# Kernel optimization log

Measured on AMD Instinct MI355X. Metric: run time of the kernel, lower is better.

Reference implementation:

```python
import jax, jax.numpy as jnp
import numpy as np

B, N, K, F, E = 2, 16384, 32, 64, 16


def setup_inputs() -> dict:
    key = jax.random.key(0)
    k1, k2, k3, k4 = jax.random.split(key, 4)
    nodes = jax.random.normal(k1, (B, N, F), dtype=jnp.float32)
    # neighbor list: for each (batch, node) a list of K neighbor node indices
    nlist = jax.random.randint(k2, (B, N, K), 0, N, dtype=jnp.int32)
    edges = jax.random.normal(k3, (B, N, K, E), dtype=jnp.float32)
    # learned weight: (node_feat, node_feat, edge_feat) as in build()
    w = jax.random.normal(k4, (F, F, E), dtype=jnp.float32) * 0.05
    return {"nodes": nodes, "nlist": nlist, "edges": edges, "w": w}


def reference(nodes, nlist, edges, w):
    # tf.gather_nd(nodes, nlist): gather neighbor features -> [B, N, K, F]
    batch_idx = jnp.arange(nodes.shape[0], dtype=nlist.dtype)[:, None, None]
    sliced = nodes[batch_idx, nlist]  # [B, N, K, F]
    # edge-conditioned contraction: edges[b,i,j,n] * sliced[b,i,j,l] * w[l,m,n]
    prod = jnp.einsum('bijn,bijl,lmn->bijm', edges, sliced, w)  # [B, N, K, F]
    # mean over the K neighbors (axis=2); activation is None
    reduced = jnp.mean(prod, axis=2)  # [B, N, F]
    return reduced
```

## Files before the change

kernel.cpp:

```cpp
#include <hip/hip_runtime.h>
#include <cstdint>
#include <cstddef>

#define LOGN 14

typedef __bf16 bf16x8 __attribute__((ext_vector_type(8)));
typedef float f32x4 __attribute__((ext_vector_type(4)));
typedef unsigned u32;

#define BARRIER() __builtin_amdgcn_s_barrier()
#define LGKM0()   __builtin_amdgcn_s_waitcnt(0xC07F)
#define SFENCE()  __builtin_amdgcn_sched_barrier(0)

__device__ __forceinline__ u32 fbits(float f) { return __builtin_bit_cast(u32, f); }
__device__ __forceinline__ u32 pkrne(float lo, float hi) {
  u32 a = fbits(lo); a = a + 0x7fffu + ((a >> 16) & 1u);
  u32 b = fbits(hi); b = b + 0x7fffu + ((b >> 16) & 1u);
  return (b & 0xffff0000u) | (a >> 16);
}


__global__ void prep_wt(const float* __restrict__ w, unsigned short* __restrict__ wt) {
  int idx = blockIdx.x * 256 + threadIdx.x;
  int m = idx >> 10, k = idx & 1023;
  int ch = k >> 3, wv = k & 7, t = ch >> 4, cc = ch & 15;
  int l = (cc << 2) + (t >> 1), n = ((t & 1) << 3) + wv;
  u32 u = fbits(w[l * 1024 + m * 16 + n] * 0.03125f);
  wt[idx] = (unsigned short)((u + 0x7fffu + ((u >> 16) & 1u)) >> 16);
}

__device__ __forceinline__ bf16x8 mk_bw(const float* wp) {
  float v[8];
  #pragma unroll
  for (int i = 0; i < 8; ++i) v[i] = wp[i] * 0.03125f;
  uint4 pk{pkrne(v[0], v[1]), pkrne(v[2], v[3]), pkrne(v[4], v[5]), pkrne(v[6], v[7])};
  return __builtin_bit_cast(bf16x8, pk);
}

template <bool USE_WT>
__global__ __launch_bounds__(256, 3)
void mp_kernel(const float* __restrict__ nodes, const int* __restrict__ nlist,
               const float* __restrict__ edges, const unsigned short* __restrict__ wt,
               const float* __restrict__ w, float* __restrict__ out) {
  __shared__ u32 g_lds[16 * 512];

  const int tid = threadIdx.x;
  const int lane = tid & 63;
  const int wid = __builtin_amdgcn_readfirstlane(tid >> 6);
  const int q = lane >> 4, c = lane & 15;

  const int blk = blockIdx.x;
  const int xcd = blk & 7;
  const int batch = xcd >> 2;
  const int ordinal = ((blk >> 3) << 2) + (xcd & 3);
  const int wg0 = (batch << LOGN) + (ordinal << 4);
  const float* __restrict__ nbase = nodes + ((size_t)batch << 20);

  const int nd0 = wid << 2;

  auto issue_nl = [&](int t, int4* ni) {
    const int* r = nlist + (((size_t)(wg0 + nd0 + t)) << 5) + (q << 3);
    ni[0] = *(const int4*)r;
    ni[1] = *(const int4*)(r + 4);
  };
  auto issue_se = [&](int t, const int4* ni, f32x4* R, float* E) {
    const int ix[8] = {ni[0].x, ni[0].y, ni[0].z, ni[0].w,
                       ni[1].x, ni[1].y, ni[1].z, ni[1].w};
    #pragma unroll
    for (int i = 0; i < 8; ++i)
      R[i] = *(const f32x4*)(nbase + ((size_t)(u32)ix[i] << 6) + (c << 2));
    const float* ep = edges + (((size_t)(wg0 + nd0 + t)) << 9) + (q << 7) + c;
    #pragma unroll
    for (int i = 0; i < 8; ++i) E[i] = ep[i << 4];
  };
  auto consume = [&](int p, const f32x4* R, const float* E) {
    uint4 apk{pkrne(E[0], E[1]), pkrne(E[2], E[3]),
              pkrne(E[4], E[5]), pkrne(E[6], E[7])};
    const bf16x8 af = __builtin_bit_cast(bf16x8, apk);
    #pragma unroll
    for (int lt = 0; lt < 4; ++lt) {
      uint4 spk{pkrne(R[0][lt], R[1][lt]), pkrne(R[2][lt], R[3][lt]),
                pkrne(R[4][lt], R[5][lt]), pkrne(R[6][lt], R[7][lt])};
      f32x4 acc{0.f, 0.f, 0.f, 0.f};
      acc = __builtin_amdgcn_mfma_f32_16x16x32_bf16(af,
              __builtin_bit_cast(bf16x8, spk), acc, 0, 0, 0);
      const u32 lo = pkrne(acc[0], acc[1]);
      const u32 hi = pkrne(acc[2], acc[3]);
      const int chunk = (c + (((lt << 1) + (q >> 1)) << 4)) ^ (p & 7);
      *(uint2*)&g_lds[(p << 9) + (chunk << 2) + ((q & 1) << 1)] = uint2{lo, hi};
    }
  };

  {
    int4 ni0[2], ni1[2];
    f32x4 R0[8], R1[8];
    float E0[8], E1[8];
    issue_nl(0, ni0);
    issue_nl(1, ni1);
    issue_se(0, ni0, R0, E0);
    issue_nl(2, ni0);
    issue_se(1, ni1, R1, E1);
    issue_nl(3, ni1);
    SFENCE();
    consume(nd0 + 0, R0, E0);
    issue_se(2, ni0, R0, E0);
    SFENCE();
    consume(nd0 + 1, R1, E1);
    issue_se(3, ni1, R1, E1);
    SFENCE();
    consume(nd0 + 2, R0, E0);
    consume(nd0 + 3, R1, E1);
  }

  LGKM0();
  BARRIER();

  const int m = (wid << 4) + c;
  f32x4 ob{0.f, 0.f, 0.f, 0.f};
  if (USE_WT) {
    const unsigned short* wb = wt + ((size_t)m << 10) + (q << 3);
    #pragma unroll 8
    for (int s = 0; s < 32; ++s) {
      uint4 ar = *(const uint4*)&g_lds[(c << 9) + ((((s << 2) + q) ^ (c & 7)) << 2)];
      ob = __builtin_amdgcn_mfma_f32_16x16x32_bf16(__builtin_bit_cast(bf16x8, ar),
                                                   *(const bf16x8*)(wb + (s << 5)),
                                                   ob, 0, 0, 0);
    }
  } else {
    #pragma unroll 4
    for (int s = 0; s < 32; ++s) {
      uint4 ar = *(const uint4*)&g_lds[(c << 9) + ((((s << 2) + q) ^ (c & 7)) << 2)];
      const int ch = (s << 2) + q;
      const int l = ((ch & 15) << 2) + (ch >> 5);
      const int n0 = ((ch >> 4) & 1) << 3;
      const float* wp = w + l * 1024 + m * 16 + n0;
      ob = __builtin_amdgcn_mfma_f32_16x16x32_bf16(__builtin_bit_cast(bf16x8, ar),
                                                   mk_bw(wp), ob, 0, 0, 0);
    }
  }

  #pragma unroll
  for (int r = 0; r < 4; ++r)
    out[((size_t)(wg0 + (q << 2) + r) << 6) + m] = ob[r];
}

extern "C" void kernel_launch(void* const* d_in, const int* in_sizes, int n_in,
                              void* d_out, int out_size, void* d_ws, size_t ws_size,
                              hipStream_t stream) {
  const float* nodes = (const float*)d_in[0];
  const int*   nlist = (const int*)d_in[1];
  const float* edges = (const float*)d_in[2];
  const float* w     = (const float*)d_in[3];
  float* out = (float*)d_out;

  if (ws_size >= 131072) {
    unsigned short* wt = (unsigned short*)d_ws;
    prep_wt<<<256, 256, 0, stream>>>(w, wt);
    mp_kernel<true><<<2048, 256, 0, stream>>>(nodes, nlist, edges, wt, w, out);
  } else {
    mp_kernel<false><<<2048, 256, 0, stream>>>(nodes, nlist, edges, nullptr, w, out);
  }
}
```

Baseline: 148.1 us.

## Pre-convert nodes to bf16 and pipeline four node-groups per persistent block

Adds a prep kernel that converts the node table to bf16 in the workspace, which halves the bytes moved by the random neighbor gathers. A new fused kernel handles 64 nodes per block in four groups, double-buffering the LDS stage so that the gathers for the next group are issued while the weight MFMAs of the current group run. Occupancy drops to 2 blocks per CU with twice the LDS, and it needs a larger workspace, which adds an extra prep launch.

```diff
diff --git a/kernel.cpp b/kernel.cpp
--- a/kernel.cpp
+++ b/kernel.cpp
@@ -29,6 +29,14 @@
   wt[idx] = (unsigned short)((u + 0x7fffu + ((u >> 16) & 1u)) >> 16);
 }
 
+__global__ void prep_nb(const float* __restrict__ nodes, unsigned short* __restrict__ nb) {
+  int idx = blockIdx.x * 256 + threadIdx.x;
+  const float4* p = (const float4*)nodes + ((size_t)idx << 1);
+  float4 a = p[0], b = p[1];
+  uint4 o{pkrne(a.x, a.y), pkrne(a.z, a.w), pkrne(b.x, b.y), pkrne(b.z, b.w)};
+  *((uint4*)nb + idx) = o;
+}
+
 __device__ __forceinline__ bf16x8 mk_bw(const float* wp) {
   float v[8];
   #pragma unroll
@@ -37,7 +45,157 @@
   return __builtin_bit_cast(bf16x8, pk);
 }
 
-template <bool USE_WT>
+__global__ __launch_bounds__(256, 2)
+void mp_fused(const int* __restrict__ nlist, const float* __restrict__ edges,
+              const unsigned short* __restrict__ wt, const unsigned short* __restrict__ nb,
+              float* __restrict__ out) {
+  __shared__ u32 g_lds[2 * 16 * 512];
+
+  const int tid = threadIdx.x;
+  const int lane = tid & 63;
+  const int wid = __builtin_amdgcn_readfirstlane(tid >> 6);
+  const int q = lane >> 4, c = lane & 15;
+
+  const int blk = blockIdx.x;
+  const int xcd = blk & 7;
+  const int batch = xcd >> 2;
+  const int ordinal = ((blk >> 3) << 2) + (xcd & 3);
+  const int wg0 = (batch << LOGN) + (ordinal << 6);
+  const unsigned short* __restrict__ nbb = nb + ((size_t)batch << 20);
+
+  const int nd0 = wid << 2;
+  const int m = (wid << 4) + c;
+  const unsigned short* __restrict__ wb = wt + ((size_t)m << 10) + (q << 3);
+
+  int4  NI[4][2];
+  uint2 U[4][8];
+  float E[4][8];
+
+  auto issue_nl = [&](int g) {
+    #pragma unroll
+    for (int j = 0; j < 4; ++j) {
+      const int* r = nlist + (((size_t)(g + nd0 + j)) << 5) + (q << 3);
+      NI[j][0] = *(const int4*)r;
+      NI[j][1] = *(const int4*)(r + 4);
+    }
+  };
+  auto issue_se2 = [&](int g, int j0) {
+    #pragma unroll
+    for (int jj = 0; jj < 2; ++jj) {
+      const int j = j0 + jj;
+      const int ix[8] = {NI[j][0].x, NI[j][0].y, NI[j][0].z, NI[j][0].w,
+                         NI[j][1].x, NI[j][1].y, NI[j][1].z, NI[j][1].w};
+      #pragma unroll
+      for (int i = 0; i < 8; ++i)
+        U[j][i] = *(const uint2*)(nbb + ((size_t)(u32)ix[i] << 6) + (c << 2));
+      const float* ep = edges + (((size_t)(g + nd0 + j)) << 9) + (q << 7) + c;
+      #pragma unroll
+      for (int i = 0; i < 8; ++i) E[j][i] = ep[i << 4];
+    }
+  };
+  auto consume_all = [&](int bsel) {
+    #pragma unroll
+    for (int j = 0; j < 4; ++j) {
+      const int p = nd0 + j;
+      uint4 apk{pkrne(E[j][0], E[j][1]), pkrne(E[j][2], E[j][3]),
+                pkrne(E[j][4], E[j][5]), pkrne(E[j][6], E[j][7])};
+      const bf16x8 af = __builtin_bit_cast(bf16x8, apk);
+      #pragma unroll
+      for (int lt = 0; lt < 4; ++lt) {
+        const u32 sel = (lt & 1) ? 0x07060302u : 0x05040100u;
+        u32 p0, p1, p2, p3;
+        if (lt & 2) {
+          p0 = __builtin_amdgcn_perm(U[j][1].y, U[j][0].y, sel);
+          p1 = __builtin_amdgcn_perm(U[j][3].y, U[j][2].y, sel);
+          p2 = __builtin_amdgcn_perm(U[j][5].y, U[j][4].y, sel);
+          p3 = __builtin_amdgcn_perm(U[j][7].y, U[j][6].y, sel);
+        } else {
+          p0 = __builtin_amdgcn_perm(U[j][1].x, U[j][0].x, sel);
+          p1 = __builtin_amdgcn_perm(U[j][3].x, U[j][2].x, sel);
+          p2 = __builtin_amdgcn_perm(U[j][5].x, U[j][4].x, sel);
+          p3 = __builtin_amdgcn_perm(U[j][7].x, U[j][6].x, sel);
+        }
+        uint4 spk{p0, p1, p2, p3};
+        f32x4 acc{0.f, 0.f, 0.f, 0.f};
+        acc = __builtin_amdgcn_mfma_f32_16x16x32_bf16(af,
+                __builtin_bit_cast(bf16x8, spk), acc, 0, 0, 0);
+        const u32 lo = pkrne(acc[0], acc[1]);
+        const u32 hi = pkrne(acc[2], acc[3]);
+        const int chunk = (c + (((lt << 1) + (q >> 1)) << 4)) ^ (p & 7);
+        *(uint2*)&g_lds[(bsel << 13) + (p << 9) + (chunk << 2) + ((q & 1) << 1)] =
+            uint2{lo, hi};
+      }
+    }
+  };
+  auto phaseB_half = [&](int bsel, int s0, f32x4& ob) {
+    #pragma unroll
+    for (int s = s0; s < s0 + 16; ++s) {
+      uint4 ar = *(const uint4*)&g_lds[(bsel << 13) + (c << 9) +
+                                       ((((s << 2) + q) ^ (c & 7)) << 2)];
+      ob = __builtin_amdgcn_mfma_f32_16x16x32_bf16(__builtin_bit_cast(bf16x8, ar),
+                                                   *(const bf16x8*)(wb + (s << 5)),
+                                                   ob, 0, 0, 0);
+    }
+  };
+  auto store_out = [&](int g, const f32x4& ob) {
+    #pragma unroll
+    for (int r = 0; r < 4; ++r)
+      out[((size_t)(g + (q << 2) + r) << 6) + m] = ob[r];
+  };
+
+  const int g0 = wg0, g1 = wg0 + 16, g2 = wg0 + 32, g3 = wg0 + 48;
+
+  issue_nl(g0);
+  issue_se2(g0, 0);
+  issue_se2(g0, 2);
+  issue_nl(g1);
+  consume_all(0);
+  LGKM0(); BARRIER();
+
+  f32x4 ob;
+
+  issue_se2(g1, 0);
+  SFENCE();
+  ob = f32x4{0.f, 0.f, 0.f, 0.f};
+  phaseB_half(0, 0, ob);
+  issue_se2(g1, 2);
+  issue_nl(g2);
+  SFENCE();
+  phaseB_half(0, 16, ob);
+  store_out(g0, ob);
+  consume_all(1);
+  LGKM0(); BARRIER();
+
+  issue_se2(g2, 0);
+  SFENCE();
+  ob = f32x4{0.f, 0.f, 0.f, 0.f};
+  phaseB_half(1, 0, ob);
+  issue_se2(g2, 2);
+  issue_nl(g3);
+  SFENCE();
+  phaseB_half(1, 16, ob);
+  store_out(g1, ob);
+  consume_all(0);
+  LGKM0(); BARRIER();
+
+  issue_se2(g3, 0);
+  SFENCE();
+  ob = f32x4{0.f, 0.f, 0.f, 0.f};
+  phaseB_half(0, 0, ob);
+  issue_se2(g3, 2);
+  SFENCE();
+  phaseB_half(0, 16, ob);
+  store_out(g2, ob);
+  consume_all(1);
+  LGKM0(); BARRIER();
+
+  ob = f32x4{0.f, 0.f, 0.f, 0.f};
+  phaseB_half(1, 0, ob);
+  phaseB_half(1, 16, ob);
+  store_out(g3, ob);
+}
+
+template <int MODE>
 __global__ __launch_bounds__(256, 3)
 void mp_kernel(const float* __restrict__ nodes, const int* __restrict__ nlist,
                const float* __restrict__ edges, const unsigned short* __restrict__ wt,
@@ -63,7 +221,7 @@
     ni[0] = *(const int4*)r;
     ni[1] = *(const int4*)(r + 4);
   };
-  auto issue_se = [&](int t, const int4* ni, f32x4* R, float* E) {
+  auto issue_se = [&](int t, const int4* ni, f32x4* R, float* Ee) {
     const int ix[8] = {ni[0].x, ni[0].y, ni[0].z, ni[0].w,
                        ni[1].x, ni[1].y, ni[1].z, ni[1].w};
     #pragma unroll
@@ -71,11 +229,11 @@
       R[i] = *(const f32x4*)(nbase + ((size_t)(u32)ix[i] << 6) + (c << 2));
     const float* ep = edges + (((size_t)(wg0 + nd0 + t)) << 9) + (q << 7) + c;
     #pragma unroll
-    for (int i = 0; i < 8; ++i) E[i] = ep[i << 4];
-  };
-  auto consume = [&](int p, const f32x4* R, const float* E) {
-    uint4 apk{pkrne(E[0], E[1]), pkrne(E[2], E[3]),
-              pkrne(E[4], E[5]), pkrne(E[6], E[7])};
+    for (int i = 0; i < 8; ++i) Ee[i] = ep[i << 4];
+  };
+  auto consume = [&](int p, const f32x4* R, const float* Ee) {
+    uint4 apk{pkrne(Ee[0], Ee[1]), pkrne(Ee[2], Ee[3]),
+              pkrne(Ee[4], Ee[5]), pkrne(Ee[6], Ee[7])};
     const bf16x8 af = __builtin_bit_cast(bf16x8, apk);
     #pragma unroll
     for (int lt = 0; lt < 4; ++lt) {
@@ -117,7 +275,7 @@
 
   const int m = (wid << 4) + c;
   f32x4 ob{0.f, 0.f, 0.f, 0.f};
-  if (USE_WT) {
+  if constexpr (MODE >= 1) {
     const unsigned short* wb = wt + ((size_t)m << 10) + (q << 3);
     #pragma unroll 8
     for (int s = 0; s < 32; ++s) {
@@ -153,11 +311,20 @@
   const float* w     = (const float*)d_in[3];
   float* out = (float*)d_out;
 
-  if (ws_size >= 131072) {
+  const size_t WT_BYTES = 131072;
+  const size_t NB_BYTES = (size_t)1 << 22;
+
+  if (ws_size >= WT_BYTES + NB_BYTES) {
+    unsigned short* wt = (unsigned short*)d_ws;
+    unsigned short* nb = wt + 65536;
+    prep_wt<<<256, 256, 0, stream>>>(w, wt);
+    prep_nb<<<1024, 256, 0, stream>>>(nodes, nb);
+    mp_fused<<<512, 256, 0, stream>>>(nlist, edges, wt, nb, out);
+  } else if (ws_size >= WT_BYTES) {
     unsigned short* wt = (unsigned short*)d_ws;
     prep_wt<<<256, 256, 0, stream>>>(w, wt);
-    mp_kernel<true><<<2048, 256, 0, stream>>>(nodes, nlist, edges, wt, w, out);
+    mp_kernel<1><<<2048, 256, 0, stream>>>(nodes, nlist, edges, wt, w, out);
   } else {
-    mp_kernel<false><<<2048, 256, 0, stream>>>(nodes, nlist, edges, nullptr, w, out);
+    mp_kernel<0><<<2048, 256, 0, stream>>>(nodes, nlist, edges, nullptr, w, out);
   }
 }
```

After: 155.3 us. 1.05x slower.
